# Kernel optimization log

Hardware: AMD Instinct MI355X
Metric: run time of the kernel (lower is better)

## Reference

```python
import jax, jax.numpy as jnp
import numpy as np

B, S, DIM = 2, 2048, 2048
H = 16
KV_RANK = 512
D_NOPE, D_ROPE, D_V = 128, 64, 128
QK_HEAD = D_NOPE + D_ROPE  # 192
THETA = 10000.0


def make_freqs(seqlen, d_rope, theta=THETA):
    inv = 1.0 / (theta ** (np.arange(0, d_rope, 2, dtype=np.float32) / d_rope))
    ang = np.outer(np.arange(seqlen, dtype=np.float32), inv)  # [S, d/2]
    return jnp.asarray(np.cos(ang)), jnp.asarray(np.sin(ang))


def apply_rope(x, cos, sin):
    # x: [b, s, h, d]; cos/sin: [s, d//2]; complex-pair rotation (interleaved pairs)
    xr = x.reshape(*x.shape[:-1], -1, 2)
    re, im = xr[..., 0], xr[..., 1]
    c = cos[None, :, None, :]
    s = sin[None, :, None, :]
    out = jnp.stack([re * c - im * s, re * s + im * c], axis=-1)
    return out.reshape(x.shape)


def setup_inputs() -> dict:
    key = jax.random.key(0)
    ks = jax.random.split(key, 6)
    w_scale = 0.02
    cos, sin = make_freqs(S, D_ROPE)
    return {
        'x': jax.random.normal(ks[0], (B, S, DIM), dtype=jnp.float32),
        'freqs_cos': cos,
        'freqs_sin': sin,
        'wq': jax.random.normal(ks[1], (H * QK_HEAD, DIM), dtype=jnp.float32) * w_scale,
        'wkv_a': jax.random.normal(ks[2], (KV_RANK + D_ROPE, DIM), dtype=jnp.float32) * w_scale,
        'wkv_b': jax.random.normal(ks[3], (H * (D_NOPE + D_V), KV_RANK), dtype=jnp.float32) * w_scale,
        'wo': jax.random.normal(ks[4], (DIM, H * D_V), dtype=jnp.float32) * w_scale,
        'alpha': jnp.ones((1,), jnp.float32) * 0.5,
        'gamma': jnp.ones((KV_RANK,), jnp.float32),
        'beta': jnp.zeros((KV_RANK,), jnp.float32),
    }


def reference(x, freqs_cos, freqs_sin, wq, wkv_a, wkv_b, wo, alpha, gamma, beta):
    b, s, _ = x.shape
    # Q projection -> [b, s, h, qk_head]
    q = (x @ wq.T).reshape(b, s, H, QK_HEAD)
    q_nope, q_pe = q[..., :D_NOPE], q[..., D_NOPE:]
    q_pe = apply_rope(q_pe, freqs_cos, freqs_sin)

    # latent KV projection
    kv_full = x @ wkv_a.T                      # [b, s, kv_rank + d_rope]
    kv, k_pe = kv_full[..., :KV_RANK], kv_full[..., KV_RANK:]
    k_pe = apply_rope(k_pe[:, :, None, :], freqs_cos, freqs_sin)[:, :, 0, :]  # [b, s, d_rope]
    # DyT norm on latent kv
    kvn = jnp.tanh(alpha * kv) * gamma + beta  # [b, s, kv_rank]

    # absorbed attention: fold wkv_b into q and output
    wkv_b_h = wkv_b.reshape(H, D_NOPE + D_V, KV_RANK)
    wk = wkv_b_h[:, :D_NOPE]                   # [h, d_nope, c]
    wv = wkv_b_h[:, D_NOPE:]                   # [h, d_v, c]
    q_abs = jnp.einsum('bshd,hdc->bshc', q_nope, wk)  # [b, s, h, c]

    scale = QK_HEAD ** -0.5
    scores = (jnp.einsum('bshc,btc->bsht', q_abs, kvn)
              + jnp.einsum('bshr,btr->bsht', q_pe, k_pe)) * scale
    probs = jax.nn.softmax(scores, axis=-1)

    o_lat = jnp.einsum('bsht,btc->bshc', probs, kvn)          # latent-space output
    o = jnp.einsum('bshc,hdc->bshd', o_lat, wv)               # [b, s, h, d_v]
    return o.reshape(b, s, H * D_V) @ wo.T
```

## Files before the change

### kernel.cpp

```cpp
#include <hip/hip_runtime.h>
#include <math.h>

typedef __bf16 bf16x8 __attribute__((ext_vector_type(8)));
typedef float f32x4 __attribute__((ext_vector_type(4)));

#define LOG2E 1.4426950408889634f

__device__ __forceinline__ unsigned short bf16r(float f) {
  unsigned u = __float_as_uint(f);
  u = (u + 0x7fffu + ((u >> 16) & 1u)) >> 16;
  return (unsigned short)u;
}
__device__ __forceinline__ unsigned short bfc(float f) {
  __bf16 h = (__bf16)f;
  return __builtin_bit_cast(unsigned short, h);
}
__device__ __forceinline__ float bf2f(unsigned short h) {
  return __uint_as_float(((unsigned)h) << 16);
}

#define GLOAD16(gsrc, ldst)                                                        \
  __builtin_amdgcn_global_load_lds(                                                \
      (const __attribute__((address_space(1))) void*)(gsrc),                       \
      (__attribute__((address_space(3))) void*)(ldst), 16, 0, 0)

__device__ __forceinline__ void map_block(int& bx, int& by, int& z) {
  const int gx = gridDim.x, gy = gridDim.y;
  const int nwg = gx * gy * gridDim.z;
  int id = blockIdx.x + gx * (blockIdx.y + gy * blockIdx.z);
  if (gridDim.z == 1 && (gx & 3) == 0 && (gy & 1) == 0 && (nwg & 7) == 0) {
    const int xcd = id & 7, k = id >> 3;
    const int rx = gx >> 2, ry = gy >> 1;
    bx = (xcd & 3) * rx + (k % rx);
    by = (xcd >> 2) * ry + (k / rx);
    z = 0;
  } else {
    if ((nwg & 7) == 0) id = (id & 7) * (nwg >> 3) + (id >> 3);
    bx = id % gx;
    const int t1 = id / gx;
    by = t1 % gy;
    z = t1 / gy;
  }
}

__global__ void conv_all(const float* __restrict__ x, const float* __restrict__ wq,
                         const float* __restrict__ wkva, const float* __restrict__ wkvb,
                         const float* __restrict__ wo,
                         unsigned short* __restrict__ xb, unsigned short* __restrict__ wqb,
                         unsigned short* __restrict__ wab, unsigned short* __restrict__ wbb,
                         unsigned short* __restrict__ wob) {
  int bid = blockIdx.x;
  const float* src; unsigned short* dst; long nsrc;
  if (bid < 8192)       {               src = x;    dst = xb;  nsrc = 8388608; }
  else if (bid < 14336) { bid -= 8192;  src = wq;   dst = wqb; nsrc = 6291456; }
  else if (bid < 15616) { bid -= 14336; src = wkva; dst = wab; nsrc = 1179648; }
  else if (bid < 17664) { bid -= 15616; src = wkvb; dst = wbb; nsrc = 2097152; }
  else                  { bid -= 17664; src = wo;   dst = wob; nsrc = 4194304; }
  long i = ((long)bid * 256 + threadIdx.x) * 4;
  ushort4 o;
  if (i < nsrc) {
    float4 v = *(const float4*)&src[i];
    o.x = bf16r(v.x); o.y = bf16r(v.y); o.z = bf16r(v.z); o.w = bf16r(v.w);
  } else {
    o.x = 0; o.y = 0; o.z = 0; o.w = 0;
  }
  *(ushort4*)&dst[i] = o;
}

template <int BN, int MODE>
__global__ __launch_bounds__(512) void gemm8p(
    const unsigned short* __restrict__ A, const unsigned short* __restrict__ B,
    void* __restrict__ Cv, float* __restrict__ laux,
    int Mrows, int K, int lda, int ldb, int ldc, int zs,
    long sAh, long sAl, long sBh, long sBl, long sCh, long sCl, float alpha)
{
  constexpr int BM = 256;
  constexpr int WN = BN / 4;
  constexpr int NR = WN / 16;
  constexpr int BU = BN / 64;
  constexpr int BU1 = (BU + 1) / 2;

  __shared__ unsigned short As[2][BM * 64];
  __shared__ unsigned short Bs[2][BN * 64];

  const int tid = threadIdx.x;
  const int w = tid >> 6, l = tid & 63, lg = l & 15, lh = l >> 4;
  const int wmi = w >> 2, wni = w & 3;
  const int lrow = l >> 3;
  const int swz8 = ((l & 7) ^ lrow) * 8;

  int bx, by, z;
  map_block(bx, by, z);
  const int zh = z >> zs, zl = z & ((1 << zs) - 1);

  const unsigned short* Ab = A + zh * sAh + zl * sAl + (long)(bx * BM) * lda;
  const unsigned short* Bb = B + zh * sBh + zl * sBl + (long)(by * BN) * ldb;

  const int nt = K >> 6;

  auto stA = [&](int T, int u) {
    if (T >= nt) return;
    const int rr = u * 64 + w * 8;
    GLOAD16(Ab + (long)(rr + lrow) * lda + (T << 6) + swz8, &As[T & 1][rr * 64]);
  };
  auto stB = [&](int T, int u) {
    if (T >= nt) return;
    const int rr = u * 64 + w * 8;
    GLOAD16(Bb + (long)(rr + lrow) * ldb + (T << 6) + swz8, &Bs[T & 1][rr * 64]);
  };

  stA(0, 0); stA(0, 1); stA(0, 2); stA(0, 3);
#pragma unroll
  for (int u = 0; u < BU; ++u) stB(0, u);
  stA(1, 0); stA(1, 2);

  f32x4 acc[8][NR] = {};

  const int nit = nt >> 1;
  for (int i = 0; i < nit; ++i) {
    const int t0 = 2 * i;
#pragma unroll
    for (int j = 0; j < 8; ++j) {
      const int tau = t0 + (j >> 2);
      const int jj = j & 3;
      const int mh = jj & 1, kh = jj >> 1;
      if (jj == 0) {
        if (tau + 1 < nt) asm volatile("s_waitcnt vmcnt(2)" ::: "memory");
        else              asm volatile("s_waitcnt vmcnt(0)" ::: "memory");
      } else {
        asm volatile("" ::: "memory");
      }
      __builtin_amdgcn_s_barrier();
      if (j == 0)      { stA(t0 + 1, 1); stA(t0 + 1, 3); }
      else if (j == 1) { for (int u = 0; u < BU1; ++u) stB(t0 + 1, u); }
      else if (j == 2) { for (int u = BU1; u < BU; ++u) stB(t0 + 1, u); }
      else if (j == 3) { stA(t0 + 2, 0); stA(t0 + 2, 2); }
      else if (j == 4) { stA(t0 + 2, 1); stA(t0 + 2, 3); }
      else if (j == 5) { for (int u = 0; u < BU1; ++u) stB(t0 + 2, u); }
      else if (j == 6) { for (int u = BU1; u < BU; ++u) stB(t0 + 2, u); }
      else             { stA(t0 + 3, 0); stA(t0 + 3, 2); }
      const unsigned short* bA = As[tau & 1];
      const unsigned short* bB = Bs[tau & 1];
      const int rswz = ((kh * 4 + lh) ^ (lg & 7)) * 8;
      bf16x8 af[4], bf[NR];
#pragma unroll
      for (int mi = 0; mi < 4; ++mi)
        af[mi] = *(const bf16x8*)&bA[(wmi * 128 + mh * 64 + mi * 16 + lg) * 64 + rswz];
#pragma unroll
      for (int ni = 0; ni < NR; ++ni)
        bf[ni] = *(const bf16x8*)&bB[(wni * WN + ni * 16 + lg) * 64 + rswz];
      __builtin_amdgcn_s_setprio(1);
#pragma unroll
      for (int mi = 0; mi < 4; ++mi)
#pragma unroll
        for (int ni = 0; ni < NR; ++ni)
          acc[mh * 4 + mi][ni] = __builtin_amdgcn_mfma_f32_16x16x32_bf16(
              af[mi], bf[ni], acc[mh * 4 + mi][ni], 0, 0, 0);
      __builtin_amdgcn_s_setprio(0);
    }
  }

  if (nt & 1) {
    const int tau = nt - 1;
    asm volatile("s_waitcnt vmcnt(0)" ::: "memory");
    __builtin_amdgcn_s_barrier();
    const unsigned short* bA = As[tau & 1];
    const unsigned short* bB = Bs[tau & 1];
#pragma unroll
    for (int jj = 0; jj < 4; ++jj) {
      const int mh = jj & 1, kh = jj >> 1;
      const int rswz = ((kh * 4 + lh) ^ (lg & 7)) * 8;
      bf16x8 af[4], bf[NR];
#pragma unroll
      for (int mi = 0; mi < 4; ++mi)
        af[mi] = *(const bf16x8*)&bA[(wmi * 128 + mh * 64 + mi * 16 + lg) * 64 + rswz];
#pragma unroll
      for (int ni = 0; ni < NR; ++ni)
        bf[ni] = *(const bf16x8*)&bB[(wni * WN + ni * 16 + lg) * 64 + rswz];
      __builtin_amdgcn_s_setprio(1);
#pragma unroll
      for (int mi = 0; mi < 4; ++mi)
#pragma unroll
        for (int ni = 0; ni < NR; ++ni)
          acc[mh * 4 + mi][ni] = __builtin_amdgcn_mfma_f32_16x16x32_bf16(
              af[mi], bf[ni], acc[mh * 4 + mi][ni], 0, 0, 0);
      __builtin_amdgcn_s_setprio(0);
    }
  }

  const int row0 = bx * BM + wmi * 128;
  const int col0 = by * BN + wni * WN;
  const long coff = (long)zh * sCh + (long)zl * sCl;

  if (MODE == 4) {
#pragma unroll
    for (int mi = 0; mi < 8; ++mi)
#pragma unroll
      for (int r = 0; r < 4; ++r) {
        const int row = row0 + mi * 16 + lh * 4 + r;
        unsigned short* dq = (unsigned short*)Cv +
            (long)(row >> 11) * 6291456 + (long)by * 393216 + (long)(row & 2047) * 192;
#pragma unroll
        for (int ni = 0; ni < NR; ++ni)
          dq[wni * WN + ni * 16 + lg] = bf16r(acc[mi][ni][r] * alpha);
      }
  } else {
#pragma unroll
    for (int mi = 0; mi < 8; ++mi)
#pragma unroll
      for (int r = 0; r < 4; ++r) {
        const int row = row0 + mi * 16 + lh * 4 + r;
#pragma unroll
        for (int ni = 0; ni < NR; ++ni) {
          float v = acc[mi][ni][r] * alpha;
          if (MODE == 0)
            ((float*)Cv)[coff + (long)row * ldc + col0 + ni * 16 + lg] = v;
          else
            ((unsigned short*)Cv)[coff + (long)row * ldc + col0 + ni * 16 + lg] = bf16r(v);
        }
      }
  }
}

template <int MODE>
__global__ __launch_bounds__(256) void gemm4w(
    const unsigned short* __restrict__ A, const unsigned short* __restrict__ B,
    void* __restrict__ Cv, float* __restrict__ laux,
    int Mrows, int K, int lda, int ldb, int ldc, int zs,
    long sAh, long sAl, long sBh, long sBl, long sCh, long sCl, float alpha)
{
  constexpr int BM = 128, BN = 128, WN = 64, NR = 4;

  __shared__ unsigned short As[2][BM * 64];
  __shared__ unsigned short Bs[2][BN * 64];

  const int tid = threadIdx.x;
  const int w = tid >> 6, l = tid & 63, lg = l & 15, lh = l >> 4;
  const int wmi = w >> 1, wni = w & 1;
  const int lrow = l >> 3;
  const int swz8 = ((l & 7) ^ lrow) * 8;

  int bx, by, z;
  map_block(bx, by, z);
  const int zh = z >> zs, zl = z & ((1 << zs) - 1);

  const unsigned short* Ab = A + zh * sAh + zl * sAl + (long)(bx * BM) * lda;
  const unsigned short* Bb = B + zh * sBh + zl * sBl + (long)(by * BN) * ldb;

  const int nt = K >> 6;

  auto stage = [&](int T) {
    const int k0 = T << 6;
    const int d = T & 1;
#pragma unroll
    for (int u = 0; u < 4; ++u) {
      const int rr = u * 32 + w * 8;
      GLOAD16(Ab + (long)(rr + lrow) * lda + k0 + swz8, &As[d][rr * 64]);
    }
#pragma unroll
    for (int u = 0; u < 4; ++u) {
      const int rr = u * 32 + w * 8;
      GLOAD16(Bb + (long)(rr + lrow) * ldb + k0 + swz8, &Bs[d][rr * 64]);
    }
  };

  f32x4 acc[4][NR] = {};

  stage(0);
  for (int t = 0; t < nt; ++t) {
    asm volatile("s_waitcnt vmcnt(0)" ::: "memory");
    __builtin_amdgcn_s_barrier();
    if (t + 1 < nt) stage(t + 1);
    const unsigned short* bA = As[t & 1];
    const unsigned short* bB = Bs[t & 1];
#pragma unroll
    for (int kh = 0; kh < 2; ++kh) {
      const int rswz = ((kh * 4 + lh) ^ (lg & 7)) * 8;
      bf16x8 af[4], bf[NR];
#pragma unroll
      for (int mi = 0; mi < 4; ++mi)
        af[mi] = *(const bf16x8*)&bA[(wmi * 64 + mi * 16 + lg) * 64 + rswz];
#pragma unroll
      for (int ni = 0; ni < NR; ++ni)
        bf[ni] = *(const bf16x8*)&bB[(wni * WN + ni * 16 + lg) * 64 + rswz];
      __builtin_amdgcn_s_setprio(1);
#pragma unroll
      for (int mi = 0; mi < 4; ++mi)
#pragma unroll
        for (int ni = 0; ni < NR; ++ni)
          acc[mi][ni] = __builtin_amdgcn_mfma_f32_16x16x32_bf16(
              af[mi], bf[ni], acc[mi][ni], 0, 0, 0);
      __builtin_amdgcn_s_setprio(0);
    }
  }

  const int row0 = bx * BM + wmi * 64;
  const int col0 = by * BN + wni * WN;
  const long coff = (long)zh * sCh + (long)zl * sCl;

#pragma unroll
  for (int mi = 0; mi < 4; ++mi)
#pragma unroll
    for (int r = 0; r < 4; ++r) {
      const int row = row0 + mi * 16 + lh * 4 + r;
#pragma unroll
      for (int ni = 0; ni < NR; ++ni) {
        float v = acc[mi][ni][r] * alpha;
        if (MODE == 0)
          ((float*)Cv)[coff + (long)row * ldc + col0 + ni * 16 + lg] = v;
        else
          ((unsigned short*)Cv)[coff + (long)row * ldc + col0 + ni * 16 + lg] = bf16r(v);
      }
    }
}

__global__ __launch_bounds__(512, 4) void attn_fused(
    const unsigned short* __restrict__ q192, const unsigned short* __restrict__ kh,
    const unsigned short* __restrict__ vhT, unsigned short* __restrict__ o_b)
{
  __shared__ unsigned short Ks[2][3 * 64 * 64];
  __shared__ unsigned short Ps[64 * 72];

  const int tid = threadIdx.x;
  const int w = tid >> 6, l = tid & 63, lg = l & 15, lh = l >> 4;
  const int wmi = w >> 2, wni = w & 3;
  const int lrow = l >> 3;
  const int swz8 = ((l & 7) ^ lrow) * 8;

  int id = blockIdx.x;
  id = (id & 7) * 128 + (id >> 3);
  const int bx = id & 31;
  const int z = id >> 5;
  const int b = z >> 4, hh = z & 15;

  const unsigned short* Qg = q192 + (long)z * 393216 + (long)(bx * 64) * 192;
  const unsigned short* Kg = kh + (long)z * 393216;
  const unsigned short* Vg = vhT + (long)z * 262144;

  bf16x8 qf[2][6];
#pragma unroll
  for (int mi = 0; mi < 2; ++mi)
#pragma unroll
    for (int s = 0; s < 6; ++s)
      qf[mi][s] = *(const bf16x8*)&Qg[(wmi * 32 + mi * 16 + lg) * 192 + s * 32 + lh * 8];

  bf16x8 ones;
#pragma unroll
  for (int j = 0; j < 8; ++j) ((unsigned short*)&ones)[j] = 0x3F80;

  auto stageK = [&](int T) {
    if (T >= 32) return;
    const unsigned short* src = Kg + (long)(T * 64) * 192;
    unsigned short* dst = Ks[T & 1];
#pragma unroll
    for (int u = 0; u < 3; ++u) {
      const int rr = w * 8;
      GLOAD16(src + (long)(rr + lrow) * 192 + u * 64 + swz8, &dst[u * 4096 + rr * 64]);
    }
  };

  f32x4 acc_o[2][2] = {};
  f32x4 accl[2] = {};

  stageK(0);
  for (int t = 0; t < 32; ++t) {
    asm volatile("s_waitcnt vmcnt(0)" ::: "memory");
    __builtin_amdgcn_s_barrier();
    bf16x8 vf[4];
#pragma unroll
    for (int j = 0; j < 4; ++j)
      vf[j] = *(const bf16x8*)&Vg[(long)(wni * 32 + (j & 1) * 16 + lg) * 2048 +
                                  t * 64 + (j >> 1) * 32 + lh * 8];
    stageK(t + 1);
    const unsigned short* bK = Ks[t & 1];

    f32x4 acc_s[2] = {};
#pragma unroll
    for (int u = 0; u < 3; ++u) {
      bf16x8 kf[2];
#pragma unroll
      for (int half = 0; half < 2; ++half) {
        const int rswz = ((half * 4 + lh) ^ (lg & 7)) * 8;
        kf[half] = *(const bf16x8*)&bK[u * 4096 + (wni * 16 + lg) * 64 + rswz];
      }
      __builtin_amdgcn_s_setprio(1);
#pragma unroll
      for (int half = 0; half < 2; ++half)
#pragma unroll
        for (int mi = 0; mi < 2; ++mi)
          acc_s[mi] = __builtin_amdgcn_mfma_f32_16x16x32_bf16(
              qf[mi][u * 2 + half], kf[half], acc_s[mi], 0, 0, 0);
      __builtin_amdgcn_s_setprio(0);
    }
#pragma unroll
    for (int mi = 0; mi < 2; ++mi)
#pragma unroll
      for (int r = 0; r < 4; ++r)
        Ps[(wmi * 32 + mi * 16 + lh * 4 + r) * 72 + wni * 16 + lg] =
            bfc(exp2f(acc_s[mi][r] * LOG2E));
    __builtin_amdgcn_s_barrier();

#pragma unroll
    for (int k2 = 0; k2 < 2; ++k2) {
      bf16x8 pf[2];
#pragma unroll
      for (int mi = 0; mi < 2; ++mi)
        pf[mi] = *(const bf16x8*)&Ps[(wmi * 32 + mi * 16 + lg) * 72 + k2 * 32 + lh * 8];
      __builtin_amdgcn_s_setprio(1);
#pragma unroll
      for (int mi = 0; mi < 2; ++mi) {
        accl[mi] = __builtin_amdgcn_mfma_f32_16x16x32_bf16(pf[mi], ones, accl[mi], 0, 0, 0);
#pragma unroll
        for (int n = 0; n < 2; ++n)
          acc_o[mi][n] = __builtin_amdgcn_mfma_f32_16x16x32_bf16(
              pf[mi], vf[k2 * 2 + n], acc_o[mi][n], 0, 0, 0);
      }
      __builtin_amdgcn_s_setprio(0);
    }
  }

#pragma unroll
  for (int mi = 0; mi < 2; ++mi)
#pragma unroll
    for (int r = 0; r < 4; ++r) {
      const int row = bx * 64 + wmi * 32 + mi * 16 + lh * 4 + r;
      const float inv = 1.0f / accl[mi][r];
      unsigned short* dst = o_b + (long)(b * 2048 + row) * 2048 + hh * 128 + wni * 32;
#pragma unroll
      for (int n = 0; n < 2; ++n)
        dst[n * 16 + lg] = bfc(acc_o[mi][n][r] * inv);
    }
}

template <int MODE>
__global__ __launch_bounds__(256) void gemm_bt2(
    const unsigned short* __restrict__ A, const unsigned short* __restrict__ B,
    void* __restrict__ Cv, float* __restrict__ laux,
    int M, int Nstore, int K, int lda, int ldb, int ldc, int zs,
    long sAh, long sAl, long sBh, long sBl, long sCh, long sCl, float alpha)
{
  __shared__ unsigned short As[128 * 32];
  __shared__ unsigned short Bs[128 * 32];
  const int tid = threadIdx.x;
  const int w = tid >> 6, l = tid & 63, lg = l & 15, lh = l >> 4;

  int bx, by, z;
  map_block(bx, by, z);

  const int zh = z >> zs, zl = z & ((1 << zs) - 1);
  const unsigned short* Ab = A + zh * sAh + zl * sAl + (long)(bx * 128) * lda;
  const unsigned short* Bb = B + zh * sBh + zl * sBl + (long)(by * 128) * ldb;
  const int srow = l >> 2;
  const int scol = (((l & 3) ^ ((l >> 3) & 3)) * 8);
  const int wm = (w >> 1) * 64, wn = (w & 1) * 64;
  f32x4 acc[4][4] = {};

  const long ra0 = (long)(w * 16 + srow) * lda + scol;
  const long ra1 = (long)(64 + w * 16 + srow) * lda + scol;
  const long rb0 = (long)(w * 16 + srow) * ldb + scol;
  const long rb1 = (long)(64 + w * 16 + srow) * ldb + scol;
  unsigned short* lA0 = &As[(w * 16) * 32];
  unsigned short* lA1 = &As[(64 + w * 16) * 32];
  unsigned short* lB0 = &Bs[(w * 16) * 32];
  unsigned short* lB1 = &Bs[(64 + w * 16) * 32];

  const int rsw = ((lh ^ ((lg >> 1) & 3)) * 8);

  for (int k0 = 0; k0 < K; k0 += 32) {
    __syncthreads();
    GLOAD16(Ab + ra0 + k0, lA0);
    GLOAD16(Ab + ra1 + k0, lA1);
    GLOAD16(Bb + rb0 + k0, lB0);
    GLOAD16(Bb + rb1 + k0, lB1);
    __syncthreads();
    bf16x8 af[4], bfr[4];
#pragma unroll
    for (int m = 0; m < 4; m++) af[m] = *(const bf16x8*)&As[(wm + m * 16 + lg) * 32 + rsw];
#pragma unroll
    for (int n = 0; n < 4; n++) bfr[n] = *(const bf16x8*)&Bs[(wn + n * 16 + lg) * 32 + rsw];
#pragma unroll
    for (int m = 0; m < 4; m++)
#pragma unroll
      for (int n = 0; n < 4; n++)
        acc[m][n] = __builtin_amdgcn_mfma_f32_16x16x32_bf16(af[m], bfr[n], acc[m][n], 0, 0, 0);
  }

  const int row0 = bx * 128 + wm, col0 = by * 128 + wn;
  long coff = zh * sCh + zl * sCl;

#pragma unroll
  for (int m = 0; m < 4; m++)
#pragma unroll
    for (int r = 0; r < 4; r++) {
      const int row = row0 + m * 16 + lh * 4 + r;
#pragma unroll
      for (int n = 0; n < 4; n++) {
        int col = col0 + n * 16 + lg;
        if (col < Nstore) {
          float v = acc[m][n][r] * alpha;
          if (MODE == 0)
            ((float*)Cv)[coff + (long)row * ldc + col] = v;
          else
            ((unsigned short*)Cv)[coff + (long)row * ldc + col] = bf16r(v);
        }
      }
    }
}

__global__ void kv_epilogue(const float* __restrict__ kvf, const float* __restrict__ fc,
                            const float* __restrict__ fs, const float* __restrict__ alpha,
                            const float* __restrict__ gamma, const float* __restrict__ beta,
                            unsigned short* __restrict__ kvn, unsigned short* __restrict__ kh) {
  const int n = blockIdx.x;
  const int b = n >> 11, s = n & 2047;
  const int tid = threadIdx.x;
  const float a = alpha[0];
  const float* src = kvf + (long)n * 576;
  unsigned short* dst = kvn + (long)n * 512;
#pragma unroll
  for (int c0 = 0; c0 < 512; c0 += 256) {
    int c = c0 + tid;
    float v = tanhf(a * src[c]) * gamma[c] + beta[c];
    dst[c] = bf16r(v);
  }
  if (tid < 32) {
    int i = tid;
    float re = src[512 + 2 * i], im = src[512 + 2 * i + 1];
    float co = fc[s * 32 + i], si = fs[s * 32 + i];
    ushort2 v;
    v.x = bf16r(re * co - im * si);
    v.y = bf16r(re * si + im * co);
#pragma unroll
    for (int h = 0; h < 16; h++)
      *(ushort2*)&kh[((long)(b * 16 + h) * 2048 + s) * 192 + 128 + 2 * i] = v;
  }
}

__global__ void q_ropefix(unsigned short* __restrict__ q192, const float* __restrict__ fc,
                          const float* __restrict__ fs) {
  const int n = blockIdx.x;
  const int b = n >> 11, s = n & 2047;
  const int tid = threadIdx.x;
  for (int it = tid; it < 512; it += 256) {
    int h = it >> 5, i = it & 31;
    unsigned short* dd = q192 + ((long)(b * 16 + h) * 2048 + s) * 192 + 128 + 2 * i;
    float re = bf2f(dd[0]), im = bf2f(dd[1]);
    float co = fc[s * 32 + i], si = fs[s * 32 + i];
    ushort2 o;
    o.x = bf16r(re * co - im * si);
    o.y = bf16r(re * si + im * co);
    *(ushort2*)dd = o;
  }
}

extern "C" void kernel_launch(void* const* d_in, const int* in_sizes, int n_in,
                              void* d_out, int out_size, void* d_ws, size_t ws_size,
                              hipStream_t stream) {
  const float* x = (const float*)d_in[0];
  const float* fc = (const float*)d_in[1];
  const float* fs = (const float*)d_in[2];
  const float* wq = (const float*)d_in[3];
  const float* wkva = (const float*)d_in[4];
  const float* wkvb = (const float*)d_in[5];
  const float* wo = (const float*)d_in[6];
  const float* alpha = (const float*)d_in[7];
  const float* gamma = (const float*)d_in[8];
  const float* beta = (const float*)d_in[9];
  float* out = (float*)d_out;

  char* p = (char*)d_ws;
  auto take = [&](size_t bytes) {
    char* r = p;
    p += (bytes + 255) & ~(size_t)255;
    return r;
  };
  unsigned short* wqb   = (unsigned short*)take(6291456ull * 2);
  float*          kvf   = (float*)take(2359296ull * 4);
  unsigned short* xb    = (unsigned short*)take(8388608ull * 2);
  unsigned short* wab   = (unsigned short*)take(1310720ull * 2);
  unsigned short* wbb   = (unsigned short*)take(2097152ull * 2);
  unsigned short* wob   = (unsigned short*)take(4194304ull * 2);
  unsigned short* kvn   = (unsigned short*)take(2097152ull * 2);
  unsigned short* kh    = (unsigned short*)take(12582912ull * 2);
  unsigned short* q192  = (unsigned short*)take(12582912ull * 2);
  unsigned short* vhT   = (unsigned short*)take(8388608ull * 2);
  unsigned short* o_b   = (unsigned short*)take(8388608ull * 2);

  const float scale = 1.0f / sqrtf(192.0f);

  conv_all<<<21760, 256, 0, stream>>>(x, wq, wkva, wkvb, wo, xb, wqb, wab, wbb, wob);

  gemm8p<192, 4><<<dim3(16, 16, 1), 512, 0, stream>>>(
      xb, wqb, q192, nullptr, 4096, 2048, 2048, 2048, 192, 0, 0, 0, 0, 0, 0, 0, scale);
  gemm_bt2<0><<<dim3(32, 5, 1), 256, 0, stream>>>(xb, wab, kvf, nullptr, 4096, 576, 2048,
                                                  2048, 2048, 576, 0, 0, 0, 0, 0, 0, 0, 1.0f);
  kv_epilogue<<<4096, 256, 0, stream>>>(kvf, fc, fs, alpha, gamma, beta, kvn, kh);
  gemm4w<1><<<dim3(16, 1, 32), 256, 0, stream>>>(
      kvn, wbb, kh, nullptr, 2048, 512, 512, 512, 192, 4,
      1048576, 0, 0, 131072, 6291456, 393216, 1.0f);
  q_ropefix<<<4096, 256, 0, stream>>>(q192, fc, fs);
  gemm4w<1><<<dim3(1, 16, 32), 256, 0, stream>>>(
      wbb + 128 * 512, kvn, vhT, nullptr, 128, 512, 512, 512, 2048, 4,
      0, 131072, 1048576, 0, 4194304, 262144, 1.0f);

  attn_fused<<<1024, 512, 0, stream>>>(q192, kh, vhT, o_b);

  gemm4w<0><<<dim3(32, 16, 1), 256, 0, stream>>>(
      o_b, wob, out, nullptr, 4096, 2048, 2048, 2048, 2048, 0,
      0, 0, 0, 0, 0, 0, 1.0f);
}
```

Before: 357.1 us.

## Software-pipeline attention loop with double-buffered P tile

```diff
diff --git a/kernel.cpp b/kernel.cpp
--- a/kernel.cpp
+++ b/kernel.cpp
@@ -319,7 +319,7 @@
     const unsigned short* __restrict__ vhT, unsigned short* __restrict__ o_b)
 {
   __shared__ unsigned short Ks[2][3 * 64 * 64];
-  __shared__ unsigned short Ps[64 * 72];
+  __shared__ unsigned short Ps[2][64 * 72];
 
   const int tid = threadIdx.x;
   const int w = tid >> 6, l = tid & 63, lg = l & 15, lh = l >> 4;
@@ -358,22 +358,40 @@
       GLOAD16(src + (long)(rr + lrow) * 192 + u * 64 + swz8, &dst[u * 4096 + rr * 64]);
     }
   };
+  auto loadV = [&](int T, bf16x8 (&vf)[4]) {
+    if (T >= 32) return;
+#pragma unroll
+    for (int j = 0; j < 4; ++j)
+      vf[j] = *(const bf16x8*)&Vg[(long)(wni * 32 + (j & 1) * 16 + lg) * 2048 +
+                                  T * 64 + (j >> 1) * 32 + lh * 8];
+  };
 
   f32x4 acc_o[2][2] = {};
   f32x4 accl[2] = {};
-
-  stageK(0);
-  for (int t = 0; t < 32; ++t) {
-    asm volatile("s_waitcnt vmcnt(0)" ::: "memory");
-    __builtin_amdgcn_s_barrier();
-    bf16x8 vf[4];
-#pragma unroll
-    for (int j = 0; j < 4; ++j)
-      vf[j] = *(const bf16x8*)&Vg[(long)(wni * 32 + (j & 1) * 16 + lg) * 2048 +
-                                  t * 64 + (j >> 1) * 32 + lh * 8];
-    stageK(t + 1);
+  bf16x8 vfA[4], vfB[4];
+
+  auto pvStep = [&](int pt, bf16x8 (&vf)[4]) {
+    const unsigned short* Pb = Ps[pt & 1];
+#pragma unroll
+    for (int k2 = 0; k2 < 2; ++k2) {
+      bf16x8 pf[2];
+#pragma unroll
+      for (int mi = 0; mi < 2; ++mi)
+        pf[mi] = *(const bf16x8*)&Pb[(wmi * 32 + mi * 16 + lg) * 72 + k2 * 32 + lh * 8];
+      __builtin_amdgcn_s_setprio(1);
+#pragma unroll
+      for (int mi = 0; mi < 2; ++mi) {
+        accl[mi] = __builtin_amdgcn_mfma_f32_16x16x32_bf16(pf[mi], ones, accl[mi], 0, 0, 0);
+#pragma unroll
+        for (int n = 0; n < 2; ++n)
+          acc_o[mi][n] = __builtin_amdgcn_mfma_f32_16x16x32_bf16(
+              pf[mi], vf[k2 * 2 + n], acc_o[mi][n], 0, 0, 0);
+      }
+      __builtin_amdgcn_s_setprio(0);
+    }
+  };
+  auto qkStep = [&](int t) {
     const unsigned short* bK = Ks[t & 1];
-
     f32x4 acc_s[2] = {};
 #pragma unroll
     for (int u = 0; u < 3; ++u) {
@@ -392,32 +410,39 @@
               qf[mi][u * 2 + half], kf[half], acc_s[mi], 0, 0, 0);
       __builtin_amdgcn_s_setprio(0);
     }
+    unsigned short* Pw = Ps[t & 1];
 #pragma unroll
     for (int mi = 0; mi < 2; ++mi)
 #pragma unroll
       for (int r = 0; r < 4; ++r)
-        Ps[(wmi * 32 + mi * 16 + lh * 4 + r) * 72 + wni * 16 + lg] =
+        Pw[(wmi * 32 + mi * 16 + lh * 4 + r) * 72 + wni * 16 + lg] =
             bfc(exp2f(acc_s[mi][r] * LOG2E));
-    __builtin_amdgcn_s_barrier();
-
-#pragma unroll
-    for (int k2 = 0; k2 < 2; ++k2) {
-      bf16x8 pf[2];
-#pragma unroll
-      for (int mi = 0; mi < 2; ++mi)
-        pf[mi] = *(const bf16x8*)&Ps[(wmi * 32 + mi * 16 + lg) * 72 + k2 * 32 + lh * 8];
-      __builtin_amdgcn_s_setprio(1);
-#pragma unroll
-      for (int mi = 0; mi < 2; ++mi) {
-        accl[mi] = __builtin_amdgcn_mfma_f32_16x16x32_bf16(pf[mi], ones, accl[mi], 0, 0, 0);
-#pragma unroll
-        for (int n = 0; n < 2; ++n)
-          acc_o[mi][n] = __builtin_amdgcn_mfma_f32_16x16x32_bf16(
-              pf[mi], vf[k2 * 2 + n], acc_o[mi][n], 0, 0, 0);
-      }
-      __builtin_amdgcn_s_setprio(0);
-    }
-  }
+  };
+
+  stageK(0);
+  for (int tt = 0; tt < 16; ++tt) {
+    {
+      const int t = 2 * tt;
+      asm volatile("s_waitcnt vmcnt(0) lgkmcnt(0)" ::: "memory");
+      __builtin_amdgcn_s_barrier();
+      stageK(t + 1);
+      loadV(t, vfA);
+      if (t > 0) pvStep(t - 1, vfB);
+      qkStep(t);
+    }
+    {
+      const int t = 2 * tt + 1;
+      asm volatile("s_waitcnt vmcnt(0) lgkmcnt(0)" ::: "memory");
+      __builtin_amdgcn_s_barrier();
+      stageK(t + 1);
+      loadV(t, vfB);
+      pvStep(t - 1, vfA);
+      qkStep(t);
+    }
+  }
+  asm volatile("s_waitcnt vmcnt(0) lgkmcnt(0)" ::: "memory");
+  __builtin_amdgcn_s_barrier();
+  pvStep(31, vfB);
 
 #pragma unroll
   for (int mi = 0; mi < 2; ++mi)
```

Result: slower. 454.8 us (+27.4%).

## Split attention over two KV halves with a separate reduction kernel

Applied to the files above, without the earlier changes.

```diff
diff --git a/kernel.cpp b/kernel.cpp
--- a/kernel.cpp
+++ b/kernel.cpp
@@ -316,7 +316,8 @@
 
 __global__ __launch_bounds__(512, 4) void attn_fused(
     const unsigned short* __restrict__ q192, const unsigned short* __restrict__ kh,
-    const unsigned short* __restrict__ vhT, unsigned short* __restrict__ o_b)
+    const unsigned short* __restrict__ vhT, float* __restrict__ o_p,
+    float* __restrict__ l_p)
 {
   __shared__ unsigned short Ks[2][3 * 64 * 64];
   __shared__ unsigned short Ps[64 * 72];
@@ -328,10 +329,12 @@
   const int swz8 = ((l & 7) ^ lrow) * 8;
 
   int id = blockIdx.x;
-  id = (id & 7) * 128 + (id >> 3);
-  const int bx = id & 31;
-  const int z = id >> 5;
-  const int b = z >> 4, hh = z & 15;
+  id = (id & 7) * 256 + (id >> 3);
+  const int half = id & 1;
+  const int bx = (id >> 1) & 31;
+  const int z = id >> 6;
+
+  const int t0 = half * 16, tend = t0 + 16;
 
   const unsigned short* Qg = q192 + (long)z * 393216 + (long)(bx * 64) * 192;
   const unsigned short* Kg = kh + (long)z * 393216;
@@ -349,7 +352,7 @@
   for (int j = 0; j < 8; ++j) ((unsigned short*)&ones)[j] = 0x3F80;
 
   auto stageK = [&](int T) {
-    if (T >= 32) return;
+    if (T >= tend) return;
     const unsigned short* src = Kg + (long)(T * 64) * 192;
     unsigned short* dst = Ks[T & 1];
 #pragma unroll
@@ -362,8 +365,8 @@
   f32x4 acc_o[2][2] = {};
   f32x4 accl[2] = {};
 
-  stageK(0);
-  for (int t = 0; t < 32; ++t) {
+  stageK(t0);
+  for (int t = t0; t < tend; ++t) {
     asm volatile("s_waitcnt vmcnt(0)" ::: "memory");
     __builtin_amdgcn_s_barrier();
     bf16x8 vf[4];
@@ -379,17 +382,17 @@
     for (int u = 0; u < 3; ++u) {
       bf16x8 kf[2];
 #pragma unroll
-      for (int half = 0; half < 2; ++half) {
-        const int rswz = ((half * 4 + lh) ^ (lg & 7)) * 8;
-        kf[half] = *(const bf16x8*)&bK[u * 4096 + (wni * 16 + lg) * 64 + rswz];
+      for (int half2 = 0; half2 < 2; ++half2) {
+        const int rswz = ((half2 * 4 + lh) ^ (lg & 7)) * 8;
+        kf[half2] = *(const bf16x8*)&bK[u * 4096 + (wni * 16 + lg) * 64 + rswz];
       }
       __builtin_amdgcn_s_setprio(1);
 #pragma unroll
-      for (int half = 0; half < 2; ++half)
+      for (int half2 = 0; half2 < 2; ++half2)
 #pragma unroll
         for (int mi = 0; mi < 2; ++mi)
           acc_s[mi] = __builtin_amdgcn_mfma_f32_16x16x32_bf16(
-              qf[mi][u * 2 + half], kf[half], acc_s[mi], 0, 0, 0);
+              qf[mi][u * 2 + half2], kf[half2], acc_s[mi], 0, 0, 0);
       __builtin_amdgcn_s_setprio(0);
     }
 #pragma unroll
@@ -419,17 +422,37 @@
     }
   }
 
+  const long zoff = ((long)(half * 32 + z)) * 2048;
 #pragma unroll
   for (int mi = 0; mi < 2; ++mi)
 #pragma unroll
     for (int r = 0; r < 4; ++r) {
       const int row = bx * 64 + wmi * 32 + mi * 16 + lh * 4 + r;
-      const float inv = 1.0f / accl[mi][r];
-      unsigned short* dst = o_b + (long)(b * 2048 + row) * 2048 + hh * 128 + wni * 32;
+      float* dst = o_p + (zoff + row) * 128 + wni * 32;
 #pragma unroll
       for (int n = 0; n < 2; ++n)
-        dst[n * 16 + lg] = bfc(acc_o[mi][n][r] * inv);
-    }
+        dst[n * 16 + lg] = acc_o[mi][n][r];
+      if (wni == 0 && lg == 0) l_p[zoff + row] = accl[mi][r];
+    }
+}
+
+__global__ void reduce_attn(const float* __restrict__ o_p, const float* __restrict__ l_p,
+                            unsigned short* __restrict__ ob) {
+  const long idx = (long)blockIdx.x * 256 + threadIdx.x;
+  const int c4 = (int)(idx & 31);
+  const int row = (int)((idx >> 5) & 2047);
+  const int z = (int)(idx >> 16);
+  const long base = ((long)z * 2048 + row) * 128 + c4 * 4;
+  float4 a = *(const float4*)&o_p[base];
+  float4 b2 = *(const float4*)&o_p[8388608 + base];
+  const float inv = 1.0f / (l_p[z * 2048 + row] + l_p[65536 + z * 2048 + row]);
+  const int b = z >> 4, hh = z & 15;
+  ushort4 o;
+  o.x = bfc((a.x + b2.x) * inv);
+  o.y = bfc((a.y + b2.y) * inv);
+  o.z = bfc((a.z + b2.z) * inv);
+  o.w = bfc((a.w + b2.w) * inv);
+  *(ushort4*)&ob[((long)(b * 2048 + row)) * 2048 + hh * 128 + c4 * 4] = o;
 }
 
 template <int MODE>
@@ -585,6 +608,8 @@
   unsigned short* q192  = (unsigned short*)take(12582912ull * 2);
   unsigned short* vhT   = (unsigned short*)take(8388608ull * 2);
   unsigned short* o_b   = (unsigned short*)take(8388608ull * 2);
+  float*          o_p   = (float*)take(16777216ull * 4);
+  float*          l_p   = (float*)take(131072ull * 4);
 
   const float scale = 1.0f / sqrtf(192.0f);
 
@@ -603,7 +628,8 @@
       wbb + 128 * 512, kvn, vhT, nullptr, 128, 512, 512, 512, 2048, 4,
       0, 131072, 1048576, 0, 4194304, 262144, 1.0f);
 
-  attn_fused<<<1024, 512, 0, stream>>>(q192, kh, vhT, o_b);
+  attn_fused<<<2048, 512, 0, stream>>>(q192, kh, vhT, o_p, l_p);
+  reduce_attn<<<8192, 256, 0, stream>>>(o_p, l_p, o_b);
 
   gemm4w<0><<<dim3(32, 16, 1), 256, 0, stream>>>(
       o_b, wob, out, nullptr, 4096, 2048, 2048, 2048, 2048, 0,
```

Result: slower. 399.5 us (+11.9%).
